# Kernel optimization log

Hardware: AMD Instinct MI355X
Metric: run time of the kernel (lower is better)

Reference implementation:

```python
import jax, jax.numpy as jnp
import numpy as np

B, S, H, KVH, D, MD = 4, 4096, 2, 1, 2, 5  # batch, seq, heads, kv heads, head_dim, model_dim
EPS, SCALE = 1e-6, 16.0


def _rmsnorm(t):
    # RMSNormNoWeight with scale=16.0 over last dim
    var = jnp.mean(t * t, axis=-1, keepdims=True)
    return SCALE * t * jax.lax.rsqrt(var + EPS)


def _rope(t, cos, sin):
    # t: (B, S, h, D); cos/sin: (S, D//2). Complex multiply on interleaved pairs.
    tr, ti = t[..., 0::2], t[..., 1::2]
    c = cos[None, :, None, :]
    s = sin[None, :, None, :]
    out_r = tr * c - ti * s
    out_i = tr * s + ti * c
    return jnp.stack([out_r, out_i], axis=-1).reshape(t.shape)


def setup_inputs() -> dict:
    key = jax.random.key(0)
    ks = jax.random.split(key, 9)
    return {
        "x": jax.random.normal(ks[0], (B, S, MD), jnp.float32),
        "freqs": jax.random.normal(ks[1], (S, D // 2), jnp.float32),
        "shared_qk_v": jax.random.normal(ks[2], (MD,), jnp.float32),
        "shared_v_v": jax.random.normal(ks[3], (MD,), jnp.float32),
        "shared_o_v": jax.random.normal(ks[4], (H * D,), jnp.float32),
        "shared_vproj_u": jax.random.normal(ks[5], (KVH * D,), jnp.float32),
        "q_u": jax.random.normal(ks[6], (H * D,), jnp.float32),
        "k_u": jax.random.normal(ks[7], (KVH * D,), jnp.float32),
        "o_u": jax.random.normal(ks[8], (MD,), jnp.float32),
    }


def reference(x, freqs, shared_qk_v, shared_v_v, shared_o_v, shared_vproj_u, q_u, k_u, o_u):
    b, s = x.shape[0], x.shape[1]
    # rank-1 projections: (x . v) outer u
    s_qk = jnp.sum(x * shared_qk_v, axis=-1, keepdims=True)  # (B,S,1) shared by q and k
    q = (s_qk * q_u).reshape(b, s, H, D)
    k = (s_qk * k_u).reshape(b, s, KVH, D)
    s_v = jnp.sum(x * shared_v_v, axis=-1, keepdims=True)
    v = (s_v * shared_vproj_u).reshape(b, s, KVH, D)
    # qk-norm + rotary
    q = _rmsnorm(q)
    k = _rmsnorm(k)
    cos, sin = jnp.cos(freqs), jnp.sin(freqs)
    q = _rope(q, cos, sin)
    k = _rope(k, cos, sin)
    # (B,h,S,D)
    q = q.transpose(0, 2, 1, 3)
    k = k.transpose(0, 2, 1, 3)
    v = v.transpose(0, 2, 1, 3)
    # GQA repeat kv heads
    k = jnp.repeat(k, H // KVH, axis=1)
    v = jnp.repeat(v, H // KVH, axis=1)
    scores = jnp.einsum('bhqd,bhkd->bhqk', q, k) / jnp.sqrt(jnp.float32(D))
    probs = jax.nn.softmax(scores, axis=-1)
    out = jnp.einsum('bhqk,bhkd->bhqd', probs, v)
    out = out.transpose(0, 2, 1, 3).reshape(b, s, H * D)
    # rank-1 output projection
    s_o = jnp.sum(out * shared_o_v, axis=-1, keepdims=True)
    return s_o * o_u  # (B,S,MODEL_DIM)
```

## Files before the change

### kernel.cpp

```cpp
#include <hip/hip_runtime.h>
#include <math.h>


#define BQ 4
#define SQ 4096
#define MDQ 5
#define EPSQ 1e-6f
#define SCALEQ 16.0f
#define L2E 1.4426950408889634f
#define ISQ2 0.70710678118654752f

typedef float v2f __attribute__((ext_vector_type(2)));

__device__ __forceinline__ float fast_exp2(float x) {
#if __has_builtin(__builtin_amdgcn_exp2f)
    return __builtin_amdgcn_exp2f(x);
#else
    return __expf(x * 0.6931471805599453f);
#endif
}

__global__ __launch_bounds__(256)
void ca_prep(const float* __restrict__ x, const float* __restrict__ freqs,
             const float* __restrict__ qk_v, const float* __restrict__ v_v,
             const float* __restrict__ k_u, float4* __restrict__ pqc)
{
    const int idx = blockIdx.x * 256 + threadIdx.x;
    const int j   = idx & (SQ - 1);

    const float w0 = k_u[0], w1 = k_u[1];
    const float mk = 0.5f * (w0 * w0 + w1 * w1);

    const float qk0 = qk_v[0], qk1 = qk_v[1], qk2 = qk_v[2], qk3 = qk_v[3], qk4 = qk_v[4];
    const float vv0 = v_v[0],  vv1 = v_v[1],  vv2 = v_v[2],  vv3 = v_v[3],  vv4 = v_v[4];

    const float* xr = x + (size_t)idx * MDQ;
    const float x0 = xr[0], x1 = xr[1], x2 = xr[2], x3 = xr[3], x4 = xr[4];
    const float a  = x0*qk0 + x1*qk1 + x2*qk2 + x3*qk3 + x4*qk4;
    const float sv = x0*vv0 + x1*vv1 + x2*vv2 + x3*vv3 + x4*vv4;

    float sj, cj;
    __sincosf(freqs[j], &sj, &cj);
    const float mu = SCALEQ * a * rsqrtf(a * a * mk + EPSQ);
    pqc[idx] = make_float4(mu * cj, mu * sj, sv, sv);
}

#define BLOCK 256
#define RSETS 4
#define RPT 2
#define ROWSB (RSETS * RPT)
#define TILES (SQ / ROWSB)
#define KTILE 256
#define NKT (SQ / KTILE)
#define JPT (KTILE / 64)

__global__ __launch_bounds__(BLOCK)
void ca_main(const float* __restrict__ x,
             const float* __restrict__ freqs,
             const float* __restrict__ qk_v,
             const float* __restrict__ o_v,
             const float* __restrict__ vproj_u,
             const float* __restrict__ q_u,
             const float* __restrict__ k_u,
             const float* __restrict__ o_u,
             const float4* __restrict__ pqc,
             float* __restrict__ out)
{
    __shared__ float4 sKey[2][KTILE];

    const int tid = threadIdx.x;
    const int sp  = tid & 63;
    const int rs  = tid >> 6;
    const int bx  = blockIdx.x;
    const int b   = bx / TILES;
    const int tile = bx % TILES;
    const int i0  = tile * ROWSB + rs * RPT;

    const float w0 = k_u[0], w1 = k_u[1];
    const float mk  = 0.5f * (w0 * w0 + w1 * w1);
    const float Mmu = SCALEQ * rsqrtf(mk);

    const float qk0 = qk_v[0], qk1 = qk_v[1], qk2 = qk_v[2], qk3 = qk_v[3], qk4 = qk_v[4];
    const float u00 = q_u[0], u01 = q_u[1], u10 = q_u[2], u11 = q_u[3];
    const float m0 = 0.5f * (u00 * u00 + u01 * u01);
    const float m1 = 0.5f * (u10 * u10 + u11 * u11);
    const float A0 = u00 * w0 + u01 * w1, B0 = u01 * w0 - u00 * w1;
    const float A1 = u10 * w0 + u11 * w1, B1 = u11 * w0 - u10 * w1;

    v2f al[RPT], be[RPT], Cc[RPT];
#pragma unroll
    for (int k = 0; k < RPT; ++k) {
        const int i = i0 + k;
        const float* xi = x + (size_t)(b * SQ + i) * MDQ;
        const float ai = xi[0]*qk0 + xi[1]*qk1 + xi[2]*qk2 + xi[3]*qk3 + xi[4]*qk4;
        float si, ci;
        __sincosf(freqs[i], &si, &ci);
        const float lam0 = SCALEQ * ai * rsqrtf(ai * ai * m0 + EPSQ);
        const float lam1 = SCALEQ * ai * rsqrtf(ai * ai * m1 + EPSQ);
        const float a0  = lam0 * (A0 * ci - B0 * si) * ISQ2;
        const float b0_ = lam0 * (A0 * si + B0 * ci) * ISQ2;
        const float a1  = lam1 * (A1 * ci - B1 * si) * ISQ2;
        const float b1_ = lam1 * (A1 * si + B1 * ci) * ISQ2;
        const float r0 = sqrtf(a0 * a0 + b0_ * b0_);
        const float r1 = sqrtf(a1 * a1 + b1_ * b1_);
        al[k] = (v2f){a0 * L2E, a1 * L2E};
        be[k] = (v2f){b0_ * L2E, b1_ * L2E};
        Cc[k] = (v2f){-r0 * Mmu * L2E, -r1 * Mmu * L2E};
    }

    const float4* __restrict__ gsrc = pqc + (size_t)b * SQ + tid;

    float4 stage = gsrc[0];
    sKey[0][tid] = stage;
    __syncthreads();

    v2f l[RPT], n[RPT];
#pragma unroll
    for (int k = 0; k < RPT; ++k) { l[k] = (v2f){0.f, 0.f}; n[k] = (v2f){0.f, 0.f}; }

    for (int t = 0; t < NKT; ++t) {
        const int cur = t & 1;
        if (t + 1 < NKT) stage = gsrc[(size_t)(t + 1) * KTILE];

        const float4* kb = &sKey[cur][sp];
#pragma unroll
        for (int jj = 0; jj < JPT; ++jj) {
            const float4 v = kb[jj * 64];
            const v2f vx = (v2f){v.x, v.x};
            const v2f vy = (v2f){v.y, v.y};
            const v2f vz = (v2f){v.z, v.w};
#pragma unroll
            for (int k = 0; k < RPT; ++k) {
                const v2f s = al[k] * vx + (be[k] * vy + Cc[k]);
                v2f e;
                e.x = fast_exp2(s.x);
                e.y = fast_exp2(s.y);
                l[k] += e;
                n[k] += e * vz;
            }
        }

        if (t + 1 < NKT) {
            sKey[cur ^ 1][tid] = stage;
            __syncthreads();
        }
    }

#pragma unroll
    for (int m = 1; m < 64; m <<= 1) {
#pragma unroll
        for (int k = 0; k < RPT; ++k) {
            l[k].x += __shfl_xor(l[k].x, m, 64);
            l[k].y += __shfl_xor(l[k].y, m, 64);
            n[k].x += __shfl_xor(n[k].x, m, 64);
            n[k].y += __shfl_xor(n[k].y, m, 64);
        }
    }

    if (sp < RPT) {
        const int k = sp;
        const float L0 = fmaxf(l[k].x, 1e-30f);
        const float L1 = fmaxf(l[k].y, 1e-30f);
        const float W0 = n[k].x / L0, W1 = n[k].y / L1;

        const float p0 = vproj_u[0], p1 = vproj_u[1];
        const float d0 = p0 * o_v[0] + p1 * o_v[1];
        const float d1 = p0 * o_v[2] + p1 * o_v[3];
        const float so = W0 * d0 + W1 * d1;

        float* orow = out + (size_t)(b * SQ + i0 + k) * MDQ;
        orow[0] = so * o_u[0];
        orow[1] = so * o_u[1];
        orow[2] = so * o_u[2];
        orow[3] = so * o_u[3];
        orow[4] = so * o_u[4];
    }
}

#define FROWS 32
#define FSPLIT 8
#define FJSUB (SQ / FSPLIT)
#define FTILES (SQ / FROWS)

__global__ __launch_bounds__(256)
void ca_fallback(const float* __restrict__ x,
                 const float* __restrict__ freqs,
                 const float* __restrict__ qk_v,
                 const float* __restrict__ v_v,
                 const float* __restrict__ o_v,
                 const float* __restrict__ vproj_u,
                 const float* __restrict__ q_u,
                 const float* __restrict__ k_u,
                 const float* __restrict__ o_u,
                 float* __restrict__ out)
{
    __shared__ float2 sPQ[SQ];
    __shared__ float  sCv[SQ];
    __shared__ float4 sRed[FROWS][FSPLIT];

    const int tid  = threadIdx.x;
    const int b    = blockIdx.x / FTILES;
    const int tile = blockIdx.x % FTILES;

    const float w0 = k_u[0], w1 = k_u[1];
    const float mk  = 0.5f * (w0 * w0 + w1 * w1);
    const float Mmu = SCALEQ * rsqrtf(mk);

    const float qk0 = qk_v[0], qk1 = qk_v[1], qk2 = qk_v[2], qk3 = qk_v[3], qk4 = qk_v[4];
    const float vv0 = v_v[0],  vv1 = v_v[1],  vv2 = v_v[2],  vv3 = v_v[3],  vv4 = v_v[4];

    for (int k = 0; k < SQ / 256; ++k) {
        const int j = tid + k * 256;
        const float* xr = x + (size_t)(b * SQ + j) * MDQ;
        const float x0 = xr[0], x1 = xr[1], x2 = xr[2], x3 = xr[3], x4 = xr[4];
        const float a  = x0*qk0 + x1*qk1 + x2*qk2 + x3*qk3 + x4*qk4;
        const float sv = x0*vv0 + x1*vv1 + x2*vv2 + x3*vv3 + x4*vv4;
        float sj, cj;
        __sincosf(freqs[j], &sj, &cj);
        const float mu = SCALEQ * a * rsqrtf(a * a * mk + EPSQ);
        sPQ[j] = make_float2(mu * cj, mu * sj);
        sCv[j] = sv;
    }

    const int row = tid & (FROWS - 1);
    const int sp  = tid / FROWS;
    const int i   = tile * FROWS + row;

    const float u00 = q_u[0], u01 = q_u[1], u10 = q_u[2], u11 = q_u[3];
    const float m0 = 0.5f * (u00 * u00 + u01 * u01);
    const float m1 = 0.5f * (u10 * u10 + u11 * u11);
    const float A0 = u00 * w0 + u01 * w1, B0 = u01 * w0 - u00 * w1;
    const float A1 = u10 * w0 + u11 * w1, B1 = u11 * w0 - u10 * w1;

    const float* xi = x + (size_t)(b * SQ + i) * MDQ;
    const float ai = xi[0]*qk0 + xi[1]*qk1 + xi[2]*qk2 + xi[3]*qk3 + xi[4]*qk4;
    float si, ci;
    __sincosf(freqs[i], &si, &ci);
    const float lam0 = SCALEQ * ai * rsqrtf(ai * ai * m0 + EPSQ);
    const float lam1 = SCALEQ * ai * rsqrtf(ai * ai * m1 + EPSQ);
    const float alr0 = lam0 * (A0 * ci - B0 * si) * ISQ2;
    const float ber0 = lam0 * (A0 * si + B0 * ci) * ISQ2;
    const float alr1 = lam1 * (A1 * ci - B1 * si) * ISQ2;
    const float ber1 = lam1 * (A1 * si + B1 * ci) * ISQ2;
    const float r0 = sqrtf(alr0 * alr0 + ber0 * ber0);
    const float r1 = sqrtf(alr1 * alr1 + ber1 * ber1);
    const float al0 = alr0 * L2E, be0 = ber0 * L2E, C0 = -r0 * Mmu * L2E;
    const float al1 = alr1 * L2E, be1 = ber1 * L2E, C1 = -r1 * Mmu * L2E;

    __syncthreads();

    const float2* __restrict__ pq  = sPQ + sp * FJSUB;
    const float*  __restrict__ cvp = sCv + sp * FJSUB;
    float l0 = 0.f, n0 = 0.f, l1 = 0.f, n1 = 0.f;
#pragma unroll 8
    for (int jj = 0; jj < FJSUB; ++jj) {
        const float2 v = pq[jj];
        const float cvx = cvp[jj];
        const float s0 = fmaf(al0, v.x, fmaf(be0, v.y, C0));
        const float s1 = fmaf(al1, v.x, fmaf(be1, v.y, C1));
        const float e0 = fast_exp2(s0);
        const float e1 = fast_exp2(s1);
        l0 += e0; n0 = fmaf(e0, cvx, n0);
        l1 += e1; n1 = fmaf(e1, cvx, n1);
    }

    sRed[row][sp] = make_float4(l0, n0, l1, n1);
    __syncthreads();

    if (tid < FROWS) {
        float L0 = 0.f, N0 = 0.f, L1 = 0.f, N1 = 0.f;
#pragma unroll
        for (int s = 0; s < FSPLIT; ++s) {
            const float4 t = sRed[tid][s];
            L0 += t.x; N0 += t.y; L1 += t.z; N1 += t.w;
        }
        L0 = fmaxf(L0, 1e-30f);
        L1 = fmaxf(L1, 1e-30f);
        const float W0 = N0 / L0, W1 = N1 / L1;
        const float p0 = vproj_u[0], p1 = vproj_u[1];
        const float d0 = p0 * o_v[0] + p1 * o_v[1];
        const float d1 = p0 * o_v[2] + p1 * o_v[3];
        const float so = W0 * d0 + W1 * d1;

        const int ig = tile * FROWS + tid;
        float* orow = out + (size_t)(b * SQ + ig) * MDQ;
        orow[0] = so * o_u[0];
        orow[1] = so * o_u[1];
        orow[2] = so * o_u[2];
        orow[3] = so * o_u[3];
        orow[4] = so * o_u[4];
    }
}

extern "C" void kernel_launch(void* const* d_in, const int* in_sizes, int n_in,
                              void* d_out, int out_size, void* d_ws, size_t ws_size,
                              hipStream_t stream) {
    (void)in_sizes; (void)n_in; (void)out_size;
    const float* x       = (const float*)d_in[0];
    const float* freqs   = (const float*)d_in[1];
    const float* qk_v    = (const float*)d_in[2];
    const float* v_v     = (const float*)d_in[3];
    const float* o_v     = (const float*)d_in[4];
    const float* vproj_u = (const float*)d_in[5];
    const float* q_u     = (const float*)d_in[6];
    const float* k_u     = (const float*)d_in[7];
    const float* o_u     = (const float*)d_in[8];
    float* out = (float*)d_out;

    const size_t pqc_bytes = (size_t)BQ * SQ * sizeof(float4);
    if (ws_size >= pqc_bytes) {
        float4* pqc = (float4*)d_ws;
        hipLaunchKernelGGL(ca_prep, dim3(BQ * SQ / 256), dim3(256), 0, stream,
                           x, freqs, qk_v, v_v, k_u, pqc);
        hipLaunchKernelGGL(ca_main, dim3(BQ * TILES), dim3(BLOCK), 0, stream,
                           x, freqs, qk_v, o_v, vproj_u, q_u, k_u, o_u, pqc, out);
    } else {
        hipLaunchKernelGGL(ca_fallback, dim3(BQ * FTILES), dim3(256), 0, stream,
                           x, freqs, qk_v, v_v, o_v, vproj_u, q_u, k_u, o_u, out);
    }
}
```

Measured before the change: 93.27 us.

## Fuse key preparation into main attention kernel and drop workspace path

Removes the separate prep kernel and the fallback kernel; each block now recomputes the projected, normalized, rotated key values and value scalars from x and freqs on the fly while staging key tiles into shared memory. This removes a kernel launch and the workspace round trip. In exchange every block redoes sincos, rsqrt and dot products for all keys, adding redundant transcendental work and uncoalesced 5-float strided loads.

```diff
diff --git a/kernel.cpp b/kernel.cpp
--- a/kernel.cpp
+++ b/kernel.cpp
@@ -20,31 +20,6 @@
 #endif
 }
 
-__global__ __launch_bounds__(256)
-void ca_prep(const float* __restrict__ x, const float* __restrict__ freqs,
-             const float* __restrict__ qk_v, const float* __restrict__ v_v,
-             const float* __restrict__ k_u, float4* __restrict__ pqc)
-{
-    const int idx = blockIdx.x * 256 + threadIdx.x;
-    const int j   = idx & (SQ - 1);
-
-    const float w0 = k_u[0], w1 = k_u[1];
-    const float mk = 0.5f * (w0 * w0 + w1 * w1);
-
-    const float qk0 = qk_v[0], qk1 = qk_v[1], qk2 = qk_v[2], qk3 = qk_v[3], qk4 = qk_v[4];
-    const float vv0 = v_v[0],  vv1 = v_v[1],  vv2 = v_v[2],  vv3 = v_v[3],  vv4 = v_v[4];
-
-    const float* xr = x + (size_t)idx * MDQ;
-    const float x0 = xr[0], x1 = xr[1], x2 = xr[2], x3 = xr[3], x4 = xr[4];
-    const float a  = x0*qk0 + x1*qk1 + x2*qk2 + x3*qk3 + x4*qk4;
-    const float sv = x0*vv0 + x1*vv1 + x2*vv2 + x3*vv3 + x4*vv4;
-
-    float sj, cj;
-    __sincosf(freqs[j], &sj, &cj);
-    const float mu = SCALEQ * a * rsqrtf(a * a * mk + EPSQ);
-    pqc[idx] = make_float4(mu * cj, mu * sj, sv, sv);
-}
-
 #define BLOCK 256
 #define RSETS 4
 #define RPT 2
@@ -55,16 +30,16 @@
 #define JPT (KTILE / 64)
 
 __global__ __launch_bounds__(BLOCK)
-void ca_main(const float* __restrict__ x,
-             const float* __restrict__ freqs,
-             const float* __restrict__ qk_v,
-             const float* __restrict__ o_v,
-             const float* __restrict__ vproj_u,
-             const float* __restrict__ q_u,
-             const float* __restrict__ k_u,
-             const float* __restrict__ o_u,
-             const float4* __restrict__ pqc,
-             float* __restrict__ out)
+void ca_fused(const float* __restrict__ x,
+              const float* __restrict__ freqs,
+              const float* __restrict__ qk_v,
+              const float* __restrict__ v_v,
+              const float* __restrict__ o_v,
+              const float* __restrict__ vproj_u,
+              const float* __restrict__ q_u,
+              const float* __restrict__ k_u,
+              const float* __restrict__ o_u,
+              float* __restrict__ out)
 {
     __shared__ float4 sKey[2][KTILE];
 
@@ -81,6 +56,7 @@
     const float Mmu = SCALEQ * rsqrtf(mk);
 
     const float qk0 = qk_v[0], qk1 = qk_v[1], qk2 = qk_v[2], qk3 = qk_v[3], qk4 = qk_v[4];
+    const float vv0 = v_v[0],  vv1 = v_v[1],  vv2 = v_v[2],  vv3 = v_v[3],  vv4 = v_v[4];
     const float u00 = q_u[0], u01 = q_u[1], u10 = q_u[2], u11 = q_u[3];
     const float m0 = 0.5f * (u00 * u00 + u01 * u01);
     const float m1 = 0.5f * (u10 * u10 + u11 * u11);
@@ -108,9 +84,21 @@
         Cc[k] = (v2f){-r0 * Mmu * L2E, -r1 * Mmu * L2E};
     }
 
-    const float4* __restrict__ gsrc = pqc + (size_t)b * SQ + tid;
+    const float* __restrict__ xb = x + (size_t)b * SQ * MDQ;
+    auto prep_key = [&](int t, float4& st) {
+        const int j = t * KTILE + tid;
+        const float* xr = xb + (size_t)j * MDQ;
+        const float x0 = xr[0], x1 = xr[1], x2 = xr[2], x3 = xr[3], x4 = xr[4];
+        const float a  = x0*qk0 + x1*qk1 + x2*qk2 + x3*qk3 + x4*qk4;
+        const float sv = x0*vv0 + x1*vv1 + x2*vv2 + x3*vv3 + x4*vv4;
+        float sj, cj;
+        __sincosf(freqs[j], &sj, &cj);
+        const float mu = SCALEQ * a * rsqrtf(a * a * mk + EPSQ);
+        st = make_float4(mu * cj, mu * sj, sv, sv);
+    };
 
-    float4 stage = gsrc[0];
+    float4 stage;
+    prep_key(0, stage);
     sKey[0][tid] = stage;
     __syncthreads();
 
@@ -120,7 +108,7 @@
 
     for (int t = 0; t < NKT; ++t) {
         const int cur = t & 1;
-        if (t + 1 < NKT) stage = gsrc[(size_t)(t + 1) * KTILE];
+        if (t + 1 < NKT) prep_key(t + 1, stage);
 
         const float4* kb = &sKey[cur][sp];
 #pragma unroll
@@ -177,125 +165,10 @@
     }
 }
 
-#define FROWS 32
-#define FSPLIT 8
-#define FJSUB (SQ / FSPLIT)
-#define FTILES (SQ / FROWS)
-
-__global__ __launch_bounds__(256)
-void ca_fallback(const float* __restrict__ x,
-                 const float* __restrict__ freqs,
-                 const float* __restrict__ qk_v,
-                 const float* __restrict__ v_v,
-                 const float* __restrict__ o_v,
-                 const float* __restrict__ vproj_u,
-                 const float* __restrict__ q_u,
-                 const float* __restrict__ k_u,
-                 const float* __restrict__ o_u,
-                 float* __restrict__ out)
-{
-    __shared__ float2 sPQ[SQ];
-    __shared__ float  sCv[SQ];
-    __shared__ float4 sRed[FROWS][FSPLIT];
-
-    const int tid  = threadIdx.x;
-    const int b    = blockIdx.x / FTILES;
-    const int tile = blockIdx.x % FTILES;
-
-    const float w0 = k_u[0], w1 = k_u[1];
-    const float mk  = 0.5f * (w0 * w0 + w1 * w1);
-    const float Mmu = SCALEQ * rsqrtf(mk);
-
-    const float qk0 = qk_v[0], qk1 = qk_v[1], qk2 = qk_v[2], qk3 = qk_v[3], qk4 = qk_v[4];
-    const float vv0 = v_v[0],  vv1 = v_v[1],  vv2 = v_v[2],  vv3 = v_v[3],  vv4 = v_v[4];
-
-    for (int k = 0; k < SQ / 256; ++k) {
-        const int j = tid + k * 256;
-        const float* xr = x + (size_t)(b * SQ + j) * MDQ;
-        const float x0 = xr[0], x1 = xr[1], x2 = xr[2], x3 = xr[3], x4 = xr[4];
-        const float a  = x0*qk0 + x1*qk1 + x2*qk2 + x3*qk3 + x4*qk4;
-        const float sv = x0*vv0 + x1*vv1 + x2*vv2 + x3*vv3 + x4*vv4;
-        float sj, cj;
-        __sincosf(freqs[j], &sj, &cj);
-        const float mu = SCALEQ * a * rsqrtf(a * a * mk + EPSQ);
-        sPQ[j] = make_float2(mu * cj, mu * sj);
-        sCv[j] = sv;
-    }
-
-    const int row = tid & (FROWS - 1);
-    const int sp  = tid / FROWS;
-    const int i   = tile * FROWS + row;
-
-    const float u00 = q_u[0], u01 = q_u[1], u10 = q_u[2], u11 = q_u[3];
-    const float m0 = 0.5f * (u00 * u00 + u01 * u01);
-    const float m1 = 0.5f * (u10 * u10 + u11 * u11);
-    const float A0 = u00 * w0 + u01 * w1, B0 = u01 * w0 - u00 * w1;
-    const float A1 = u10 * w0 + u11 * w1, B1 = u11 * w0 - u10 * w1;
-
-    const float* xi = x + (size_t)(b * SQ + i) * MDQ;
-    const float ai = xi[0]*qk0 + xi[1]*qk1 + xi[2]*qk2 + xi[3]*qk3 + xi[4]*qk4;
-    float si, ci;
-    __sincosf(freqs[i], &si, &ci);
-    const float lam0 = SCALEQ * ai * rsqrtf(ai * ai * m0 + EPSQ);
-    const float lam1 = SCALEQ * ai * rsqrtf(ai * ai * m1 + EPSQ);
-    const float alr0 = lam0 * (A0 * ci - B0 * si) * ISQ2;
-    const float ber0 = lam0 * (A0 * si + B0 * ci) * ISQ2;
-    const float alr1 = lam1 * (A1 * ci - B1 * si) * ISQ2;
-    const float ber1 = lam1 * (A1 * si + B1 * ci) * ISQ2;
-    const float r0 = sqrtf(alr0 * alr0 + ber0 * ber0);
-    const float r1 = sqrtf(alr1 * alr1 + ber1 * ber1);
-    const float al0 = alr0 * L2E, be0 = ber0 * L2E, C0 = -r0 * Mmu * L2E;
-    const float al1 = alr1 * L2E, be1 = ber1 * L2E, C1 = -r1 * Mmu * L2E;
-
-    __syncthreads();
-
-    const float2* __restrict__ pq  = sPQ + sp * FJSUB;
-    const float*  __restrict__ cvp = sCv + sp * FJSUB;
-    float l0 = 0.f, n0 = 0.f, l1 = 0.f, n1 = 0.f;
-#pragma unroll 8
-    for (int jj = 0; jj < FJSUB; ++jj) {
-        const float2 v = pq[jj];
-        const float cvx = cvp[jj];
-        const float s0 = fmaf(al0, v.x, fmaf(be0, v.y, C0));
-        const float s1 = fmaf(al1, v.x, fmaf(be1, v.y, C1));
-        const float e0 = fast_exp2(s0);
-        const float e1 = fast_exp2(s1);
-        l0 += e0; n0 = fmaf(e0, cvx, n0);
-        l1 += e1; n1 = fmaf(e1, cvx, n1);
-    }
-
-    sRed[row][sp] = make_float4(l0, n0, l1, n1);
-    __syncthreads();
-
-    if (tid < FROWS) {
-        float L0 = 0.f, N0 = 0.f, L1 = 0.f, N1 = 0.f;
-#pragma unroll
-        for (int s = 0; s < FSPLIT; ++s) {
-            const float4 t = sRed[tid][s];
-            L0 += t.x; N0 += t.y; L1 += t.z; N1 += t.w;
-        }
-        L0 = fmaxf(L0, 1e-30f);
-        L1 = fmaxf(L1, 1e-30f);
-        const float W0 = N0 / L0, W1 = N1 / L1;
-        const float p0 = vproj_u[0], p1 = vproj_u[1];
-        const float d0 = p0 * o_v[0] + p1 * o_v[1];
-        const float d1 = p0 * o_v[2] + p1 * o_v[3];
-        const float so = W0 * d0 + W1 * d1;
-
-        const int ig = tile * FROWS + tid;
-        float* orow = out + (size_t)(b * SQ + ig) * MDQ;
-        orow[0] = so * o_u[0];
-        orow[1] = so * o_u[1];
-        orow[2] = so * o_u[2];
-        orow[3] = so * o_u[3];
-        orow[4] = so * o_u[4];
-    }
-}
-
 extern "C" void kernel_launch(void* const* d_in, const int* in_sizes, int n_in,
                               void* d_out, int out_size, void* d_ws, size_t ws_size,
                               hipStream_t stream) {
-    (void)in_sizes; (void)n_in; (void)out_size;
+    (void)in_sizes; (void)n_in; (void)out_size; (void)d_ws; (void)ws_size;
     const float* x       = (const float*)d_in[0];
     const float* freqs   = (const float*)d_in[1];
     const float* qk_v    = (const float*)d_in[2];
@@ -307,15 +180,6 @@
     const float* o_u     = (const float*)d_in[8];
     float* out = (float*)d_out;
 
-    const size_t pqc_bytes = (size_t)BQ * SQ * sizeof(float4);
-    if (ws_size >= pqc_bytes) {
-        float4* pqc = (float4*)d_ws;
-        hipLaunchKernelGGL(ca_prep, dim3(BQ * SQ / 256), dim3(256), 0, stream,
-                           x, freqs, qk_v, v_v, k_u, pqc);
-        hipLaunchKernelGGL(ca_main, dim3(BQ * TILES), dim3(BLOCK), 0, stream,
-                           x, freqs, qk_v, o_v, vproj_u, q_u, k_u, o_u, pqc, out);
-    } else {
-        hipLaunchKernelGGL(ca_fallback, dim3(BQ * FTILES), dim3(256), 0, stream,
-                           x, freqs, qk_v, v_v, o_v, vproj_u, q_u, k_u, o_u, out);
-    }
+    hipLaunchKernelGGL(ca_fused, dim3(BQ * TILES), dim3(BLOCK), 0, stream,
+                       x, freqs, qk_v, v_v, o_v, vproj_u, q_u, k_u, o_u, out);
 }
```

Measured after the change: 99.82 us. 7.0% more time.
